# Performance work log

Measured on AMD Instinct MI355X. Metric: run time of the kernel, lower is better.

## Reference

```python
import jax, jax.numpy as jnp
import numpy as np

BIN_NUM = [16, 8, 4, 2, 1]
WIDTH_TOKEN_NUM = 4


def setup_inputs() -> dict:
    key = jax.random.key(0)
    x = jax.random.normal(key, (32, 256, 32, 16, 16), dtype=jnp.float32)
    return {"x": x}


def reference(x) -> jnp.ndarray:
    # x: [n, c, s, h, w] -> out: [n, c, s, sum(bin_num), k]
    n, c, s, h, w = x.shape
    k = WIDTH_TOKEN_NUM
    feats = []
    for b in BIN_NUM:
        # split height into b bins of size h//b, reduce with mean+max
        z = x.reshape(n, c, s, b, h // b, w)
        z = jnp.mean(z, axis=-2) + jnp.max(z, axis=-2)  # [n, c, s, b, w]
        # adaptive avg+max pool over width to k tokens (w divisible by k -> exact bins)
        z = z.reshape(n, c, s, b, k, w // k)
        z = jnp.mean(z, axis=-1) + jnp.max(z, axis=-1)  # [n, c, s, b, k]
        feats.append(z)
    return jnp.concatenate(feats, axis=3)
```

## Files before the change

kernel.cpp:

```cpp
#include <hip/hip_runtime.h>


__global__ __launch_bounds__(256) void hwtp_kernel(const float* __restrict__ x,
                                                   float* __restrict__ out,
                                                   int num_slices) {
    const int gtid  = blockIdx.x * blockDim.x + threadIdx.x;
    const int slice = gtid >> 6;
    const int lane  = threadIdx.x & 63;
    if (slice >= num_slices) return;

    const float4 v = reinterpret_cast<const float4*>(x)[(size_t)slice * 64 + lane];
    float* __restrict__ o = out + (size_t)slice * 124;

    const int g = lane & 3;

    float s0 = v.x, s1 = v.y, s2 = v.z, s3 = v.w;
    float m0 = v.x, m1 = v.y, m2 = v.z, m3 = v.w;

    {
        float z0 = s0 + m0, z1 = s1 + m1, z2 = s2 + m2, z3 = s3 + m3;
        float val = 0.25f * ((z0 + z1) + (z2 + z3))
                  + fmaxf(fmaxf(z0, z1), fmaxf(z2, z3));
        o[lane] = val;
    }

#define REDUCE(mask)                                                     \
    s0 += __shfl_xor(s0, mask); s1 += __shfl_xor(s1, mask);              \
    s2 += __shfl_xor(s2, mask); s3 += __shfl_xor(s3, mask);              \
    m0 = fmaxf(m0, __shfl_xor(m0, mask));                                \
    m1 = fmaxf(m1, __shfl_xor(m1, mask));                                \
    m2 = fmaxf(m2, __shfl_xor(m2, mask));                                \
    m3 = fmaxf(m3, __shfl_xor(m3, mask));

#define TOKEN_VAL(inv_span, dst)                                         \
    {                                                                    \
        float z0 = fmaf(s0, inv_span, m0);                               \
        float z1 = fmaf(s1, inv_span, m1);                               \
        float z2 = fmaf(s2, inv_span, m2);                               \
        float z3 = fmaf(s3, inv_span, m3);                               \
        dst = 0.25f * ((z0 + z1) + (z2 + z3))                            \
            + fmaxf(fmaxf(z0, z1), fmaxf(z2, z3));                       \
    }

    float val;

    REDUCE(4)
    TOKEN_VAL(0.5f, val)
    if ((lane & 4) == 0)
        o[64 + ((lane >> 3) << 2) + g] = val;

    REDUCE(8)
    TOKEN_VAL(0.25f, val)
    if ((lane & 12) == 0)
        o[96 + ((lane >> 4) << 2) + g] = val;

    REDUCE(16)
    TOKEN_VAL(0.125f, val)
    if ((lane & 28) == 0)
        o[112 + ((lane >> 5) << 2) + g] = val;

    REDUCE(32)
    TOKEN_VAL(0.0625f, val)
    if (lane < 4)
        o[120 + g] = val;

#undef REDUCE
#undef TOKEN_VAL
}

extern "C" void kernel_launch(void* const* d_in, const int* in_sizes, int n_in,
                              void* d_out, int out_size, void* d_ws, size_t ws_size,
                              hipStream_t stream) {
    const float* x = (const float*)d_in[0];
    float* out = (float*)d_out;

    const int num_slices = in_sizes[0] / 256;
    const int block = 256;
    const int grid = (num_slices * 64 + block - 1) / block;

    hwtp_kernel<<<grid, block, 0, stream>>>(x, out, num_slices);
}
```

Before: 376.5 us.

## Use persistent grid-stride waves with next-slice prefetch and nontemporal stores

Result: slower. 426.5 us (+13.3%).

```diff
diff --git a/kernel.cpp b/kernel.cpp
--- a/kernel.cpp
+++ b/kernel.cpp
@@ -4,68 +4,82 @@
 __global__ __launch_bounds__(256) void hwtp_kernel(const float* __restrict__ x,
                                                    float* __restrict__ out,
                                                    int num_slices) {
-    const int gtid  = blockIdx.x * blockDim.x + threadIdx.x;
-    const int slice = gtid >> 6;
-    const int lane  = threadIdx.x & 63;
+    const int lane      = threadIdx.x & 63;
+    const int wave_id   = (blockIdx.x * blockDim.x + threadIdx.x) >> 6;
+    const int num_waves = (gridDim.x * blockDim.x) >> 6;
+    const int g         = lane & 3;
+
+    const float4* __restrict__ xv = reinterpret_cast<const float4*>(x);
+
+    int slice = wave_id;
     if (slice >= num_slices) return;
 
-    const float4 v = reinterpret_cast<const float4*>(x)[(size_t)slice * 64 + lane];
-    float* __restrict__ o = out + (size_t)slice * 124;
+    float4 v = xv[(size_t)slice * 64 + lane];
 
-    const int g = lane & 3;
+    while (slice < num_slices) {
+        const int next = slice + num_waves;
+        float4 vn = make_float4(0.f, 0.f, 0.f, 0.f);
+        if (next < num_slices)
+            vn = xv[(size_t)next * 64 + lane];
 
-    float s0 = v.x, s1 = v.y, s2 = v.z, s3 = v.w;
-    float m0 = v.x, m1 = v.y, m2 = v.z, m3 = v.w;
+        float* __restrict__ o = out + (size_t)slice * 124;
 
-    {
-        float z0 = s0 + m0, z1 = s1 + m1, z2 = s2 + m2, z3 = s3 + m3;
-        float val = 0.25f * ((z0 + z1) + (z2 + z3))
-                  + fmaxf(fmaxf(z0, z1), fmaxf(z2, z3));
-        o[lane] = val;
-    }
+        float s0 = v.x, s1 = v.y, s2 = v.z, s3 = v.w;
+        float m0 = v.x, m1 = v.y, m2 = v.z, m3 = v.w;
+
+        {
+            float z0 = s0 + m0, z1 = s1 + m1, z2 = s2 + m2, z3 = s3 + m3;
+            float val = 0.25f * ((z0 + z1) + (z2 + z3))
+                      + fmaxf(fmaxf(z0, z1), fmaxf(z2, z3));
+            __builtin_nontemporal_store(val, &o[lane]);
+        }
 
 #define REDUCE(mask)                                                     \
-    s0 += __shfl_xor(s0, mask); s1 += __shfl_xor(s1, mask);              \
-    s2 += __shfl_xor(s2, mask); s3 += __shfl_xor(s3, mask);              \
-    m0 = fmaxf(m0, __shfl_xor(m0, mask));                                \
-    m1 = fmaxf(m1, __shfl_xor(m1, mask));                                \
-    m2 = fmaxf(m2, __shfl_xor(m2, mask));                                \
-    m3 = fmaxf(m3, __shfl_xor(m3, mask));
+        s0 += __shfl_xor(s0, mask); s1 += __shfl_xor(s1, mask);          \
+        s2 += __shfl_xor(s2, mask); s3 += __shfl_xor(s3, mask);          \
+        m0 = fmaxf(m0, __shfl_xor(m0, mask));                            \
+        m1 = fmaxf(m1, __shfl_xor(m1, mask));                            \
+        m2 = fmaxf(m2, __shfl_xor(m2, mask));                            \
+        m3 = fmaxf(m3, __shfl_xor(m3, mask));
 
 #define TOKEN_VAL(inv_span, dst)                                         \
-    {                                                                    \
-        float z0 = fmaf(s0, inv_span, m0);                               \
-        float z1 = fmaf(s1, inv_span, m1);                               \
-        float z2 = fmaf(s2, inv_span, m2);                               \
-        float z3 = fmaf(s3, inv_span, m3);                               \
-        dst = 0.25f * ((z0 + z1) + (z2 + z3))                            \
-            + fmaxf(fmaxf(z0, z1), fmaxf(z2, z3));                       \
-    }
+        {                                                                \
+            float z0 = fmaf(s0, inv_span, m0);                           \
+            float z1 = fmaf(s1, inv_span, m1);                           \
+            float z2 = fmaf(s2, inv_span, m2);                           \
+            float z3 = fmaf(s3, inv_span, m3);                           \
+            dst = 0.25f * ((z0 + z1) + (z2 + z3))                        \
+                + fmaxf(fmaxf(z0, z1), fmaxf(z2, z3));                   \
+        }
 
-    float val;
+        float val;
 
-    REDUCE(4)
-    TOKEN_VAL(0.5f, val)
-    if ((lane & 4) == 0)
-        o[64 + ((lane >> 3) << 2) + g] = val;
+        REDUCE(4)
+        TOKEN_VAL(0.5f, val)
+        if ((lane & 4) == 0)
+            __builtin_nontemporal_store(val, &o[64 + ((lane >> 3) << 2) + g]);
 
-    REDUCE(8)
-    TOKEN_VAL(0.25f, val)
-    if ((lane & 12) == 0)
-        o[96 + ((lane >> 4) << 2) + g] = val;
+        REDUCE(8)
+        TOKEN_VAL(0.25f, val)
+        if ((lane & 12) == 0)
+            __builtin_nontemporal_store(val, &o[96 + ((lane >> 4) << 2) + g]);
 
-    REDUCE(16)
-    TOKEN_VAL(0.125f, val)
-    if ((lane & 28) == 0)
-        o[112 + ((lane >> 5) << 2) + g] = val;
+        REDUCE(16)
+        TOKEN_VAL(0.125f, val)
+        if ((lane & 28) == 0)
+            __builtin_nontemporal_store(val, &o[112 + ((lane >> 5) << 2) + g]);
 
-    REDUCE(32)
-    TOKEN_VAL(0.0625f, val)
-    if (lane < 4)
-        o[120 + g] = val;
+        REDUCE(32)
+        TOKEN_VAL(0.0625f, val)
+        if (lane < 4)
+            __builtin_nontemporal_store(val, &o[120 + g]);
 
 #undef REDUCE
 #undef TOKEN_VAL
+
+        v = vn;
+        slice = next;
+    }
 }
 
 extern "C" void kernel_launch(void* const* d_in, const int* in_sizes, int n_in,
@@ -75,8 +89,11 @@
     float* out = (float*)d_out;
 
     const int num_slices = in_sizes[0] / 256;
+
     const int block = 256;
-    const int grid = (num_slices * 64 + block - 1) / block;
+    int grid = 2048;
+    const int max_grid = (num_slices * 64 + block - 1) / block;
+    if (grid > max_grid) grid = max_grid;
 
     hwtp_kernel<<<grid, block, 0, stream>>>(x, out, num_slices);
 }
```

## Assign each slice to sixteen lanes with register-resident rows instead of wave shuffles

Applied to the files above, without the earlier changes.

Result: slower. 432.1 us (+14.8%).

```diff
diff --git a/kernel.cpp b/kernel.cpp
--- a/kernel.cpp
+++ b/kernel.cpp
@@ -1,71 +1,77 @@
 #include <hip/hip_runtime.h>
 
+
+__device__ __forceinline__ float4 add4(float4 a, float4 b) {
+    return make_float4(a.x + b.x, a.y + b.y, a.z + b.z, a.w + b.w);
+}
+__device__ __forceinline__ float4 max4(float4 a, float4 b) {
+    return make_float4(fmaxf(a.x, b.x), fmaxf(a.y, b.y),
+                       fmaxf(a.z, b.z), fmaxf(a.w, b.w));
+}
+__device__ __forceinline__ float hsum(float4 a) {
+    return (a.x + a.y) + (a.z + a.w);
+}
+__device__ __forceinline__ float hmax(float4 a) {
+    return fmaxf(fmaxf(a.x, a.y), fmaxf(a.z, a.w));
+}
+__device__ __forceinline__ float token_val(float4 s, float4 m, float inv_span) {
+    float4 z = make_float4(fmaf(s.x, inv_span, m.x), fmaf(s.y, inv_span, m.y),
+                           fmaf(s.z, inv_span, m.z), fmaf(s.w, inv_span, m.w));
+    return fmaf(hsum(z), 0.25f, hmax(z));
+}
 
 __global__ __launch_bounds__(256) void hwtp_kernel(const float* __restrict__ x,
                                                    float* __restrict__ out,
                                                    int num_slices) {
-    const int gtid  = blockIdx.x * blockDim.x + threadIdx.x;
-    const int slice = gtid >> 6;
-    const int lane  = threadIdx.x & 63;
+    const int lane = threadIdx.x & 63;
+    const int wave = (blockIdx.x * blockDim.x + threadIdx.x) >> 6;
+    const int s    = lane >> 2;
+    const int g    = lane & 3;
+    const int slice = wave * 16 + s;
     if (slice >= num_slices) return;
 
-    const float4 v = reinterpret_cast<const float4*>(x)[(size_t)slice * 64 + lane];
+    const float4* __restrict__ xv = reinterpret_cast<const float4*>(x);
+    const size_t base = (size_t)slice * 64 + g;
+
+    float4 row[16];
+#pragma unroll
+    for (int r = 0; r < 16; ++r)
+        row[r] = xv[base + (size_t)(r * 4)];
+
     float* __restrict__ o = out + (size_t)slice * 124;
 
-    const int g = lane & 3;
+    float4 s4, m4, s8, m8, s16, m16;
 
-    float s0 = v.x, s1 = v.y, s2 = v.z, s3 = v.w;
-    float m0 = v.x, m1 = v.y, m2 = v.z, m3 = v.w;
+#pragma unroll
+    for (int j = 0; j < 8; ++j) {
+        const float4 a = row[2 * j];
+        const float4 b = row[2 * j + 1];
 
-    {
-        float z0 = s0 + m0, z1 = s1 + m1, z2 = s2 + m2, z3 = s3 + m3;
-        float val = 0.25f * ((z0 + z1) + (z2 + z3))
-                  + fmaxf(fmaxf(z0, z1), fmaxf(z2, z3));
-        o[lane] = val;
+        o[(2 * j) * 4 + g]     = fmaf(hsum(a), 0.5f, 2.0f * hmax(a));
+        o[(2 * j + 1) * 4 + g] = fmaf(hsum(b), 0.5f, 2.0f * hmax(b));
+
+        const float4 ps = add4(a, b);
+        const float4 pm = max4(a, b);
+        o[64 + j * 4 + g] = token_val(ps, pm, 0.5f);
+
+        if ((j & 1) == 0) { s4 = ps; m4 = pm; }
+        else {
+            s4 = add4(s4, ps); m4 = max4(m4, pm);
+            o[96 + (j >> 1) * 4 + g] = token_val(s4, m4, 0.25f);
+
+            if ((j & 3) == 1) { s8 = s4; m8 = m4; }
+            else {
+                s8 = add4(s8, s4); m8 = max4(m8, m4);
+                o[112 + (j >> 2) * 4 + g] = token_val(s8, m8, 0.125f);
+
+                if (j == 3) { s16 = s8; m16 = m8; }
+                else {
+                    s16 = add4(s16, s8); m16 = max4(m16, m8);
+                    o[120 + g] = token_val(s16, m16, 0.0625f);
+                }
+            }
+        }
     }
-
-#define REDUCE(mask)                                                     \
-    s0 += __shfl_xor(s0, mask); s1 += __shfl_xor(s1, mask);              \
-    s2 += __shfl_xor(s2, mask); s3 += __shfl_xor(s3, mask);              \
-    m0 = fmaxf(m0, __shfl_xor(m0, mask));                                \
-    m1 = fmaxf(m1, __shfl_xor(m1, mask));                                \
-    m2 = fmaxf(m2, __shfl_xor(m2, mask));                                \
-    m3 = fmaxf(m3, __shfl_xor(m3, mask));
-
-#define TOKEN_VAL(inv_span, dst)                                         \
-    {                                                                    \
-        float z0 = fmaf(s0, inv_span, m0);                               \
-        float z1 = fmaf(s1, inv_span, m1);                               \
-        float z2 = fmaf(s2, inv_span, m2);                               \
-        float z3 = fmaf(s3, inv_span, m3);                               \
-        dst = 0.25f * ((z0 + z1) + (z2 + z3))                            \
-            + fmaxf(fmaxf(z0, z1), fmaxf(z2, z3));                       \
-    }
-
-    float val;
-
-    REDUCE(4)
-    TOKEN_VAL(0.5f, val)
-    if ((lane & 4) == 0)
-        o[64 + ((lane >> 3) << 2) + g] = val;
-
-    REDUCE(8)
-    TOKEN_VAL(0.25f, val)
-    if ((lane & 12) == 0)
-        o[96 + ((lane >> 4) << 2) + g] = val;
-
-    REDUCE(16)
-    TOKEN_VAL(0.125f, val)
-    if ((lane & 28) == 0)
-        o[112 + ((lane >> 5) << 2) + g] = val;
-
-    REDUCE(32)
-    TOKEN_VAL(0.0625f, val)
-    if (lane < 4)
-        o[120 + g] = val;
-
-#undef REDUCE
-#undef TOKEN_VAL
 }
 
 extern "C" void kernel_launch(void* const* d_in, const int* in_sizes, int n_in,
@@ -75,8 +81,10 @@
     float* out = (float*)d_out;
 
     const int num_slices = in_sizes[0] / 256;
+
     const int block = 256;
-    const int grid = (num_slices * 64 + block - 1) / block;
+    const int slices_per_block = 64;
+    const int grid = (num_slices + slices_per_block - 1) / slices_per_block;
 
     hwtp_kernel<<<grid, block, 0, stream>>>(x, out, num_slices);
 }
```
